# Optimization experiments

Measured on AMD Instinct MI355X. Metric: run time of the kernel, lower is better.

The kernel has to match this reference:

```python
import jax, jax.numpy as jnp
import numpy as np
import itertools

F = 3          # num_sparse_features
C = 256        # num_categories
D = 64         # embedding_dim
H = 1024       # hidden_units
ND = 13        # num_dense_features
B = 16384      # batch
COMBOS = [c for r in range(2, F + 1) for c in itertools.combinations(range(F), r)]
WIDE_DIM = C * F + sum(C ** len(c) for c in COMBOS) + ND
DEEP_IN = F * D + ND


def setup_inputs() -> dict:
    key = jax.random.key(0)
    ks = jax.random.split(key, 12)
    sparse_inputs = jax.random.randint(ks[0], (B, F), 0, C, dtype=jnp.int32)
    dense_inputs = jax.random.normal(ks[1], (B, ND), dtype=jnp.float32)
    wide_w = jax.random.normal(ks[2], (WIDE_DIM,), dtype=jnp.float32) * 0.01
    wide_b = jax.random.normal(ks[3], (1,), dtype=jnp.float32) * 0.01
    emb = jax.random.normal(ks[4], (F, C, D), dtype=jnp.float32) * 0.05
    W1 = jax.random.normal(ks[5], (H, DEEP_IN), dtype=jnp.float32) / np.sqrt(DEEP_IN).astype(np.float32)
    b1 = jnp.zeros((H,), jnp.float32)
    W2 = jax.random.normal(ks[6], (H, H), dtype=jnp.float32) / np.sqrt(H).astype(np.float32)
    b2 = jnp.zeros((H,), jnp.float32)
    W3 = jax.random.normal(ks[7], (1, H), dtype=jnp.float32) / np.sqrt(H).astype(np.float32)
    b3 = jnp.zeros((1,), jnp.float32)
    return {"sparse_inputs": sparse_inputs, "dense_inputs": dense_inputs,
            "wide_w": wide_w, "wide_b": wide_b, "emb": emb,
            "W1": W1, "b1": b1, "W2": W2, "b2": b2, "W3": W3, "b3": b3}


def reference(sparse_inputs, dense_inputs, wide_w, wide_b, emb, W1, b1, W2, b2, W3, b3):
    # Wide path: one_hot(x) @ W.T  ==  gather of W columns at the hot indices.
    wide = wide_b[0]  # scalar, broadcasts to [B]
    for i in range(F):  # per-feature one-hot block, width C each
        wide = wide + wide_w[i * C + sparse_inputs[:, i]]
    off = F * C
    for combo in COMBOS:  # cross-feature one-hot blocks, width C**len(combo)
        cross = sparse_inputs[:, combo[0]]
        for j in combo[1:]:
            # faithful to source: multiplies by num_sparse_features (F), not C
            cross = cross * F + sparse_inputs[:, j]
        wide = wide + wide_w[off + cross]
        off += C ** len(combo)
    wide = wide + dense_inputs @ wide_w[off:off + ND]  # dense tail of wide linear
    wide = wide[:, None]  # [B, 1]

    # Deep path: per-feature embedding lookup -> concat -> 3-layer MLP
    embedded = jnp.concatenate([emb[i][sparse_inputs[:, i]] for i in range(F)], axis=1)  # [B, F*D]
    deep_x = jnp.concatenate([embedded, dense_inputs], axis=1)  # [B, DEEP_IN]
    h = jax.nn.relu(deep_x @ W1.T + b1)
    h = jax.nn.relu(h @ W2.T + b2)
    deep = h @ W3.T + b3  # [B, 1]

    return jax.nn.sigmoid(wide + deep)
```

## Files before the change

kernel.cpp:

```cpp
#include <hip/hip_runtime.h>
#include <stdint.h>


#define BATCH 16384
#define HDIM 1024
#define KPAD 256
#define DEEP_IN 205

typedef short bf16x8 __attribute__((ext_vector_type(8)));
typedef float f32x4 __attribute__((ext_vector_type(4)));
typedef uint16_t u16x8 __attribute__((ext_vector_type(8)));

__device__ __forceinline__ float bf2f(uint16_t u) {
    uint32_t x = ((uint32_t)u) << 16;
    float f;
    __builtin_memcpy(&f, &x, 4);
    return f;
}

__device__ __forceinline__ uint16_t f2bf(float f) {
    uint32_t x;
    __builtin_memcpy(&x, &f, 4);
    uint32_t r = (x + 0x7fffu + ((x >> 16) & 1u)) >> 16;
    return (uint16_t)r;
}

__device__ __forceinline__ void async_ld16(const uint16_t* g, uint16_t* l) {
    __builtin_amdgcn_global_load_lds(
        (const __attribute__((address_space(1))) uint32_t*)g,
        (__attribute__((address_space(3))) uint32_t*)l, 16, 0, 0);
}

__global__ __launch_bounds__(256) void prep_kernel(
    const int* __restrict__ sp, const float* __restrict__ dense,
    const float* __restrict__ emb,
    const float* __restrict__ W1, const float* __restrict__ W2,
    const float* __restrict__ ww, const float* __restrict__ wb,
    uint16_t* __restrict__ dx, uint16_t* __restrict__ W1b,
    uint16_t* __restrict__ W2b, float* __restrict__ wide)
{
    const int bid = blockIdx.x;
    if (bid < 2048) {
        int idx = bid * 256 + threadIdx.x;
        int b = idx >> 5, c0 = (idx & 31) * 8;
        u16x8 o;
        if (c0 < 192) {
            int f = c0 >> 6, cc = c0 & 63;
            int s = sp[b * 3 + f];
            const float* e = emb + (size_t)(((f << 8) + s) * 64 + cc);
            float4 v0 = *(const float4*)e;
            float4 v1 = *(const float4*)(e + 4);
            o[0] = f2bf(v0.x); o[1] = f2bf(v0.y); o[2] = f2bf(v0.z); o[3] = f2bf(v0.w);
            o[4] = f2bf(v1.x); o[5] = f2bf(v1.y); o[6] = f2bf(v1.z); o[7] = f2bf(v1.w);
        } else {
#pragma unroll
            for (int t = 0; t < 8; t++) {
                int c = c0 + t;
                o[t] = (c >= 192 && c < DEEP_IN) ? f2bf(dense[b * 13 + (c - 192)])
                                                 : (uint16_t)0;
            }
        }
        *(u16x8*)(dx + (size_t)idx * 8) = o;
    } else if (bid < 2560) {
        int k = (bid - 2048) * 256 + threadIdx.x;
        const float* src = W2 + (size_t)k * 8;
        float4 v0 = *(const float4*)src;
        float4 v1 = *(const float4*)(src + 4);
        u16x8 o;
        o[0] = f2bf(v0.x); o[1] = f2bf(v0.y); o[2] = f2bf(v0.z); o[3] = f2bf(v0.w);
        o[4] = f2bf(v1.x); o[5] = f2bf(v1.y); o[6] = f2bf(v1.z); o[7] = f2bf(v1.w);
        *(u16x8*)(W2b + (size_t)k * 8) = o;
    } else if (bid < 2688) {
        int idx = (bid - 2560) * 256 + threadIdx.x;
        int n = idx >> 5, c0 = (idx & 31) * 8;
        u16x8 o;
#pragma unroll
        for (int t = 0; t < 8; t++) {
            int c = c0 + t;
            o[t] = (c < DEEP_IN) ? f2bf(W1[n * DEEP_IN + c]) : (uint16_t)0;
        }
        *(u16x8*)(W1b + (size_t)idx * 8) = o;
    } else {
        int b = (bid - 2688) * 256 + threadIdx.x;
        int s0 = sp[b * 3], s1 = sp[b * 3 + 1], s2 = sp[b * 3 + 2];
        float w = wb[0];
        w += ww[s0] + ww[256 + s1] + ww[512 + s2];
        w += ww[768    + s0 * 3 + s1];
        w += ww[66304  + s0 * 3 + s2];
        w += ww[131840 + s1 * 3 + s2];
        w += ww[197376 + (s0 * 3 + s1) * 3 + s2];
        const float* wd = ww + 16974592;
        float acc = 0.f;
#pragma unroll
        for (int j = 0; j < 13; j++) acc += dense[b * 13 + j] * wd[j];
        wide[b] = w + acc;
    }
}

__global__ __launch_bounds__(1024, 4) void gemm_bt(
    const uint16_t* __restrict__ A, const uint16_t* __restrict__ Bw,
    const float* __restrict__ bias, uint16_t* __restrict__ C,
    int M, int N, int K, int relu)
{
    __shared__ __align__(16) uint16_t Al[2][8192];
    __shared__ __align__(16) uint16_t Bl[2][8192];

    const int tid = threadIdx.x;
    const int lane = tid & 63;
    const int wave = tid >> 6;
    const int wm = wave >> 2;
    const int wn = wave & 3;

    const int id = blockIdx.x;
    const int xcd = id & 7;
    const int slot = id >> 3;
    const int mb8 = (M >> 8) >> 3;
    const int by = xcd * mb8 + (slot >> 2);
    const int bx = slot & 3;
    const int bm = by * 256;
    const int bn = bx * 256;
    const int rl = lane & 15, q = lane >> 4;

    f32x4 acc[4][4];
#pragma unroll
    for (int i = 0; i < 4; i++)
#pragma unroll
        for (int j = 0; j < 4; j++) acc[i][j] = (f32x4)0.f;

    const uint16_t* aS = A + (size_t)(bm + wave * 16 + rl) * K + q * 8;
    const uint16_t* bS = Bw + (size_t)(bn + wave * 16 + rl) * K + q * 8;
    const int dOf = wave * 512;

    async_ld16(aS, &Al[0][dOf]);
    async_ld16(bS, &Bl[0][dOf]);
    asm volatile("s_waitcnt vmcnt(0)" ::: "memory");
    __syncthreads();

    int p = 0;
    for (int k0 = 32; k0 < K; k0 += 32) {
        async_ld16(aS + k0, &Al[p ^ 1][dOf]);
        async_ld16(bS + k0, &Bl[p ^ 1][dOf]);

        bf16x8 af[4], bfr[4];
#pragma unroll
        for (int i = 0; i < 4; i++)
            af[i] = *(const bf16x8*)&Al[p][(wm * 4 + i) * 512 + lane * 8];
#pragma unroll
        for (int j = 0; j < 4; j++)
            bfr[j] = *(const bf16x8*)&Bl[p][(wn * 4 + j) * 512 + lane * 8];
#pragma unroll
        for (int i = 0; i < 4; i++)
#pragma unroll
            for (int j = 0; j < 4; j++)
                acc[i][j] = __builtin_amdgcn_mfma_f32_16x16x32_bf16(
                    af[i], bfr[j], acc[i][j], 0, 0, 0);

        asm volatile("s_waitcnt vmcnt(0)" ::: "memory");
        __syncthreads();
        p ^= 1;
    }

    {
        bf16x8 af[4], bfr[4];
#pragma unroll
        for (int i = 0; i < 4; i++)
            af[i] = *(const bf16x8*)&Al[p][(wm * 4 + i) * 512 + lane * 8];
#pragma unroll
        for (int j = 0; j < 4; j++)
            bfr[j] = *(const bf16x8*)&Bl[p][(wn * 4 + j) * 512 + lane * 8];
#pragma unroll
        for (int i = 0; i < 4; i++)
#pragma unroll
            for (int j = 0; j < 4; j++)
                acc[i][j] = __builtin_amdgcn_mfma_f32_16x16x32_bf16(
                    af[i], bfr[j], acc[i][j], 0, 0, 0);
    }

#pragma unroll
    for (int i = 0; i < 4; i++) {
#pragma unroll
        for (int j = 0; j < 4; j++) {
            int n = bn + (wn * 4 + j) * 16 + rl;
            float bv = bias[n];
#pragma unroll
            for (int r = 0; r < 4; r++) {
                int m = bm + (wm * 4 + i) * 16 + q * 4 + r;
                float v = acc[i][j][r] + bv;
                if (relu) v = fmaxf(v, 0.f);
                C[(size_t)m * N + n] = f2bf(v);
            }
        }
    }
}

__global__ __launch_bounds__(256) void final_kernel(
    const uint16_t* __restrict__ h2, const float* __restrict__ W3,
    const float* __restrict__ b3, const float* __restrict__ wide,
    float* __restrict__ out)
{
    int wave = threadIdx.x >> 6, lane = threadIdx.x & 63;
    int row = blockIdx.x * 4 + wave;
    const uint16_t* hr = h2 + (size_t)row * HDIM + lane * 16;
    u16x8 h0 = *(const u16x8*)hr;
    u16x8 h1 = *(const u16x8*)(hr + 8);
    const float* w3 = W3 + lane * 16;
    float s = 0.f;
#pragma unroll
    for (int t = 0; t < 8; t++) s += bf2f(h0[t]) * w3[t];
#pragma unroll
    for (int t = 0; t < 8; t++) s += bf2f(h1[t]) * w3[8 + t];
#pragma unroll
    for (int off = 32; off; off >>= 1) s += __shfl_down(s, off, 64);
    if (lane == 0) {
        float x = s + wide[row] + b3[0];
        out[row] = 1.f / (1.f + __expf(-x));
    }
}

extern "C" void kernel_launch(void* const* d_in, const int* in_sizes, int n_in,
                              void* d_out, int out_size, void* d_ws, size_t ws_size,
                              hipStream_t stream) {
    const int*   sp    = (const int*)d_in[0];
    const float* dense = (const float*)d_in[1];
    const float* ww    = (const float*)d_in[2];
    const float* wb    = (const float*)d_in[3];
    const float* emb   = (const float*)d_in[4];
    const float* W1    = (const float*)d_in[5];
    const float* b1    = (const float*)d_in[6];
    const float* W2    = (const float*)d_in[7];
    const float* b2    = (const float*)d_in[8];
    const float* W3    = (const float*)d_in[9];
    const float* b3    = (const float*)d_in[10];
    float* out = (float*)d_out;

    char* ws = (char*)d_ws;
    float*    wide = (float*)ws;
    uint16_t* dxp  = (uint16_t*)(ws + 65536);
    uint16_t* W1b  = (uint16_t*)(ws + 8454144);
    uint16_t* W2b  = (uint16_t*)(ws + 8978432);
    uint16_t* h1   = (uint16_t*)(ws + 11075584);
    uint16_t* h2   = (uint16_t*)(ws + 44630016);

    prep_kernel<<<2752, 256, 0, stream>>>(sp, dense, emb, W1, W2, ww, wb,
                                          dxp, W1b, W2b, wide);
    gemm_bt<<<(BATCH / 256) * 4, 1024, 0, stream>>>(
        dxp, W1b, b1, h1, BATCH, HDIM, KPAD, 1);
    gemm_bt<<<(BATCH / 256) * 4, 1024, 0, stream>>>(
        h1, W2b, b2, h2, BATCH, HDIM, HDIM, 1);
    final_kernel<<<BATCH / 4, 256, 0, stream>>>(h2, W3, b3, wide, out);
}
```

Before: 191.6 us.

## Fuse embedding gather into first GEMM and final projection into second GEMM epilogue

Removes the separate prep, first-GEMM, and final kernels. The first kernel now gathers embeddings, dense features and W1 straight into LDS as bf16 and computes layer 1 with K trimmed to 224. It also converts W2 and computes the wide term with b3 folded in. The second GEMM uses 128x256 tiles with 512 threads and folds relu, the W3 dot product and atomics into a per-row accumulator, so h2 is never written. A last-block counter then applies the sigmoid. This saves launches and the dx/h2 round trips, at the cost of float atomics, an uncoalesced W1 gather repeated per block, and a single block doing the final pass.

```diff
diff --git a/kernel.cpp b/kernel.cpp
--- a/kernel.cpp
+++ b/kernel.cpp
@@ -4,19 +4,12 @@
 
 #define BATCH 16384
 #define HDIM 1024
-#define KPAD 256
+#define K1 224
 #define DEEP_IN 205
 
 typedef short bf16x8 __attribute__((ext_vector_type(8)));
 typedef float f32x4 __attribute__((ext_vector_type(4)));
 typedef uint16_t u16x8 __attribute__((ext_vector_type(8)));
-
-__device__ __forceinline__ float bf2f(uint16_t u) {
-    uint32_t x = ((uint32_t)u) << 16;
-    float f;
-    __builtin_memcpy(&f, &x, 4);
-    return f;
-}
 
 __device__ __forceinline__ uint16_t f2bf(float f) {
     uint32_t x;
@@ -31,78 +24,151 @@
         (__attribute__((address_space(3))) uint32_t*)l, 16, 0, 0);
 }
 
-__global__ __launch_bounds__(256) void prep_kernel(
+__global__ __launch_bounds__(512, 4) void mega1(
     const int* __restrict__ sp, const float* __restrict__ dense,
-    const float* __restrict__ emb,
-    const float* __restrict__ W1, const float* __restrict__ W2,
+    const float* __restrict__ emb, const float* __restrict__ W1,
+    const float* __restrict__ b1, const float* __restrict__ W2,
     const float* __restrict__ ww, const float* __restrict__ wb,
-    uint16_t* __restrict__ dx, uint16_t* __restrict__ W1b,
-    uint16_t* __restrict__ W2b, float* __restrict__ wide)
+    const float* __restrict__ b3,
+    uint16_t* __restrict__ h1, uint16_t* __restrict__ W2b,
+    float* __restrict__ wide, unsigned* __restrict__ cnt)
 {
     const int bid = blockIdx.x;
-    if (bid < 2048) {
-        int idx = bid * 256 + threadIdx.x;
-        int b = idx >> 5, c0 = (idx & 31) * 8;
-        u16x8 o;
-        if (c0 < 192) {
-            int f = c0 >> 6, cc = c0 & 63;
-            int s = sp[b * 3 + f];
-            const float* e = emb + (size_t)(((f << 8) + s) * 64 + cc);
-            float4 v0 = *(const float4*)e;
-            float4 v1 = *(const float4*)(e + 4);
+    const int tid = threadIdx.x;
+
+    if (bid >= 512) {
+        if (bid < 768) {
+            int k = (bid - 512) * 512 + tid;
+            const float* src = W2 + (size_t)k * 8;
+            float4 v0 = *(const float4*)src;
+            float4 v1 = *(const float4*)(src + 4);
+            u16x8 o;
             o[0] = f2bf(v0.x); o[1] = f2bf(v0.y); o[2] = f2bf(v0.z); o[3] = f2bf(v0.w);
             o[4] = f2bf(v1.x); o[5] = f2bf(v1.y); o[6] = f2bf(v1.z); o[7] = f2bf(v1.w);
+            *(u16x8*)(W2b + (size_t)k * 8) = o;
         } else {
-#pragma unroll
-            for (int t = 0; t < 8; t++) {
-                int c = c0 + t;
-                o[t] = (c >= 192 && c < DEEP_IN) ? f2bf(dense[b * 13 + (c - 192)])
-                                                 : (uint16_t)0;
+            int b = (bid - 768) * 512 + tid;
+            int s0 = sp[b * 3], s1 = sp[b * 3 + 1], s2 = sp[b * 3 + 2];
+            float w = wb[0] + b3[0];
+            w += ww[s0] + ww[256 + s1] + ww[512 + s2];
+            w += ww[768    + s0 * 3 + s1];
+            w += ww[66304  + s0 * 3 + s2];
+            w += ww[131840 + s1 * 3 + s2];
+            w += ww[197376 + (s0 * 3 + s1) * 3 + s2];
+            const float* wd = ww + 16974592;
+            float acc = 0.f;
+#pragma unroll
+            for (int j = 0; j < 13; j++) acc += dense[b * 13 + j] * wd[j];
+            wide[b] = w + acc;
+            if (bid == 768 && tid == 0) *cnt = 0u;
+        }
+        return;
+    }
+
+    __shared__ __align__(16) uint16_t Al[4096];
+    __shared__ __align__(16) uint16_t Bl[8192];
+
+    const int lane = tid & 63;
+    const int wave = tid >> 6;
+    const int wm = wave >> 2;
+    const int wn = wave & 3;
+    const int xcd = bid & 7;
+    const int slot = bid >> 3;
+    const int by = xcd * 16 + (slot >> 2);
+    const int bx = slot & 3;
+    const int bm = by * 128;
+    const int bn = bx * 256;
+    const int rl = lane & 15, q = lane >> 4;
+
+    const int rA = bm + wave * 16 + rl;
+    const int s0 = sp[rA * 3], s1 = sp[rA * 3 + 1], s2 = sp[rA * 3 + 2];
+    const float* e0 = emb + (size_t)s0 * 64;
+    const float* e1 = emb + (size_t)(256 + s1) * 64;
+    const float* e2 = emb + (size_t)(512 + s2) * 64;
+    const float* dA = dense + (size_t)rA * 13;
+    const int n0 = bn + (2 * wave) * 16 + rl;
+    const float* w10 = W1 + (size_t)n0 * 205;
+    const float* w11 = w10 + (size_t)16 * 205;
+
+    f32x4 acc[4][4];
+#pragma unroll
+    for (int i = 0; i < 4; i++)
+#pragma unroll
+        for (int j = 0; j < 4; j++) acc[i][j] = (f32x4)0.f;
+
+    u16x8 a8, bb0, bb1;
+
+#define BUILD(K0)                                                              \
+    {                                                                          \
+        int x = (K0) + q * 8;                                                  \
+        if (x < 192) {                                                         \
+            const float* e = (x < 64) ? (e0 + x)                               \
+                           : (x < 128) ? (e1 + (x - 64)) : (e2 + (x - 128));   \
+            float4 v0 = *(const float4*)e;                                     \
+            float4 v1 = *(const float4*)(e + 4);                               \
+            a8[0] = f2bf(v0.x); a8[1] = f2bf(v0.y);                            \
+            a8[2] = f2bf(v0.z); a8[3] = f2bf(v0.w);                            \
+            a8[4] = f2bf(v1.x); a8[5] = f2bf(v1.y);                            \
+            a8[6] = f2bf(v1.z); a8[7] = f2bf(v1.w);                            \
+        } else {                                                               \
+            _Pragma("unroll") for (int t = 0; t < 8; t++) {                    \
+                int c = x + t;                                                 \
+                a8[t] = (c < DEEP_IN) ? f2bf(dA[c - 192]) : (uint16_t)0;       \
+            }                                                                  \
+        }                                                                      \
+        _Pragma("unroll") for (int t = 0; t < 8; t++) {                        \
+            int c = x + t;                                                     \
+            bb0[t] = (c < DEEP_IN) ? f2bf(w10[c]) : (uint16_t)0;               \
+            bb1[t] = (c < DEEP_IN) ? f2bf(w11[c]) : (uint16_t)0;               \
+        }                                                                      \
+    }
+
+    BUILD(0)
+    for (int k0 = 0; k0 < K1; k0 += 32) {
+        __syncthreads();
+        *(u16x8*)&Al[wave * 512 + lane * 8] = a8;
+        *(u16x8*)&Bl[(2 * wave) * 512 + lane * 8] = bb0;
+        *(u16x8*)&Bl[(2 * wave + 1) * 512 + lane * 8] = bb1;
+        __syncthreads();
+        if (k0 + 32 < K1) BUILD(k0 + 32)
+        bf16x8 af[4], bfr[4];
+#pragma unroll
+        for (int i = 0; i < 4; i++)
+            af[i] = *(const bf16x8*)&Al[(wm * 4 + i) * 512 + lane * 8];
+#pragma unroll
+        for (int j = 0; j < 4; j++)
+            bfr[j] = *(const bf16x8*)&Bl[(wn * 4 + j) * 512 + lane * 8];
+#pragma unroll
+        for (int i = 0; i < 4; i++)
+#pragma unroll
+            for (int j = 0; j < 4; j++)
+                acc[i][j] = __builtin_amdgcn_mfma_f32_16x16x32_bf16(
+                    af[i], bfr[j], acc[i][j], 0, 0, 0);
+    }
+#undef BUILD
+
+#pragma unroll
+    for (int i = 0; i < 4; i++) {
+#pragma unroll
+        for (int j = 0; j < 4; j++) {
+            int n = bn + (wn * 4 + j) * 16 + rl;
+            float bv = b1[n];
+#pragma unroll
+            for (int r = 0; r < 4; r++) {
+                int m = bm + (wm * 4 + i) * 16 + q * 4 + r;
+                h1[(size_t)m * HDIM + n] = f2bf(fmaxf(acc[i][j][r] + bv, 0.f));
             }
         }
-        *(u16x8*)(dx + (size_t)idx * 8) = o;
-    } else if (bid < 2560) {
-        int k = (bid - 2048) * 256 + threadIdx.x;
-        const float* src = W2 + (size_t)k * 8;
-        float4 v0 = *(const float4*)src;
-        float4 v1 = *(const float4*)(src + 4);
-        u16x8 o;
-        o[0] = f2bf(v0.x); o[1] = f2bf(v0.y); o[2] = f2bf(v0.z); o[3] = f2bf(v0.w);
-        o[4] = f2bf(v1.x); o[5] = f2bf(v1.y); o[6] = f2bf(v1.z); o[7] = f2bf(v1.w);
-        *(u16x8*)(W2b + (size_t)k * 8) = o;
-    } else if (bid < 2688) {
-        int idx = (bid - 2560) * 256 + threadIdx.x;
-        int n = idx >> 5, c0 = (idx & 31) * 8;
-        u16x8 o;
-#pragma unroll
-        for (int t = 0; t < 8; t++) {
-            int c = c0 + t;
-            o[t] = (c < DEEP_IN) ? f2bf(W1[n * DEEP_IN + c]) : (uint16_t)0;
-        }
-        *(u16x8*)(W1b + (size_t)idx * 8) = o;
-    } else {
-        int b = (bid - 2688) * 256 + threadIdx.x;
-        int s0 = sp[b * 3], s1 = sp[b * 3 + 1], s2 = sp[b * 3 + 2];
-        float w = wb[0];
-        w += ww[s0] + ww[256 + s1] + ww[512 + s2];
-        w += ww[768    + s0 * 3 + s1];
-        w += ww[66304  + s0 * 3 + s2];
-        w += ww[131840 + s1 * 3 + s2];
-        w += ww[197376 + (s0 * 3 + s1) * 3 + s2];
-        const float* wd = ww + 16974592;
-        float acc = 0.f;
-#pragma unroll
-        for (int j = 0; j < 13; j++) acc += dense[b * 13 + j] * wd[j];
-        wide[b] = w + acc;
-    }
-}
-
-__global__ __launch_bounds__(1024, 4) void gemm_bt(
+    }
+}
+
+__global__ __launch_bounds__(512, 4) void gemm2(
     const uint16_t* __restrict__ A, const uint16_t* __restrict__ Bw,
-    const float* __restrict__ bias, uint16_t* __restrict__ C,
-    int M, int N, int K, int relu)
+    const float* __restrict__ bias, const float* __restrict__ W3,
+    float* __restrict__ outacc, float* __restrict__ out,
+    unsigned* __restrict__ cnt)
 {
-    __shared__ __align__(16) uint16_t Al[2][8192];
+    __shared__ __align__(16) uint16_t Al[2][4096];
     __shared__ __align__(16) uint16_t Bl[2][8192];
 
     const int tid = threadIdx.x;
@@ -110,16 +176,15 @@
     const int wave = tid >> 6;
     const int wm = wave >> 2;
     const int wn = wave & 3;
-
     const int id = blockIdx.x;
     const int xcd = id & 7;
     const int slot = id >> 3;
-    const int mb8 = (M >> 8) >> 3;
-    const int by = xcd * mb8 + (slot >> 2);
+    const int by = xcd * 16 + (slot >> 2);
     const int bx = slot & 3;
-    const int bm = by * 256;
+    const int bm = by * 128;
     const int bn = bx * 256;
     const int rl = lane & 15, q = lane >> 4;
+    const int K = HDIM;
 
     f32x4 acc[4][4];
 #pragma unroll
@@ -128,18 +193,21 @@
         for (int j = 0; j < 4; j++) acc[i][j] = (f32x4)0.f;
 
     const uint16_t* aS = A + (size_t)(bm + wave * 16 + rl) * K + q * 8;
-    const uint16_t* bS = Bw + (size_t)(bn + wave * 16 + rl) * K + q * 8;
-    const int dOf = wave * 512;
-
-    async_ld16(aS, &Al[0][dOf]);
-    async_ld16(bS, &Bl[0][dOf]);
+    const uint16_t* bS0 = Bw + (size_t)(bn + wave * 32 + rl) * K + q * 8;
+    const uint16_t* bS1 = bS0 + (size_t)16 * K;
+    const int dA = wave * 512, dB0 = wave * 1024, dB1 = wave * 1024 + 512;
+
+    async_ld16(aS, &Al[0][dA]);
+    async_ld16(bS0, &Bl[0][dB0]);
+    async_ld16(bS1, &Bl[0][dB1]);
     asm volatile("s_waitcnt vmcnt(0)" ::: "memory");
     __syncthreads();
 
     int p = 0;
     for (int k0 = 32; k0 < K; k0 += 32) {
-        async_ld16(aS + k0, &Al[p ^ 1][dOf]);
-        async_ld16(bS + k0, &Bl[p ^ 1][dOf]);
+        async_ld16(aS + k0, &Al[p ^ 1][dA]);
+        async_ld16(bS0 + k0, &Bl[p ^ 1][dB0]);
+        async_ld16(bS1 + k0, &Bl[p ^ 1][dB1]);
 
         bf16x8 af[4], bfr[4];
 #pragma unroll
@@ -159,7 +227,6 @@
         __syncthreads();
         p ^= 1;
     }
-
     {
         bf16x8 af[4], bfr[4];
 #pragma unroll
@@ -176,44 +243,46 @@
                     af[i], bfr[j], acc[i][j], 0, 0, 0);
     }
 
+    float bv[4], w3v[4];
+#pragma unroll
+    for (int j = 0; j < 4; j++) {
+        int n = bn + (wn * 4 + j) * 16 + rl;
+        bv[j] = bias[n];
+        w3v[j] = W3[n];
+    }
 #pragma unroll
     for (int i = 0; i < 4; i++) {
 #pragma unroll
-        for (int j = 0; j < 4; j++) {
-            int n = bn + (wn * 4 + j) * 16 + rl;
-            float bv = bias[n];
-#pragma unroll
-            for (int r = 0; r < 4; r++) {
+        for (int r = 0; r < 4; r++) {
+            float pt = 0.f;
+#pragma unroll
+            for (int j = 0; j < 4; j++)
+                pt += fmaxf(acc[i][j][r] + bv[j], 0.f) * w3v[j];
+            pt += __shfl_xor(pt, 1);
+            pt += __shfl_xor(pt, 2);
+            pt += __shfl_xor(pt, 4);
+            pt += __shfl_xor(pt, 8);
+            if (rl == 0) {
                 int m = bm + (wm * 4 + i) * 16 + q * 4 + r;
-                float v = acc[i][j][r] + bv;
-                if (relu) v = fmaxf(v, 0.f);
-                C[(size_t)m * N + n] = f2bf(v);
+                atomicAdd(&outacc[m], pt);
             }
         }
     }
-}
-
-__global__ __launch_bounds__(256) void final_kernel(
-    const uint16_t* __restrict__ h2, const float* __restrict__ W3,
-    const float* __restrict__ b3, const float* __restrict__ wide,
-    float* __restrict__ out)
-{
-    int wave = threadIdx.x >> 6, lane = threadIdx.x & 63;
-    int row = blockIdx.x * 4 + wave;
-    const uint16_t* hr = h2 + (size_t)row * HDIM + lane * 16;
-    u16x8 h0 = *(const u16x8*)hr;
-    u16x8 h1 = *(const u16x8*)(hr + 8);
-    const float* w3 = W3 + lane * 16;
-    float s = 0.f;
-#pragma unroll
-    for (int t = 0; t < 8; t++) s += bf2f(h0[t]) * w3[t];
-#pragma unroll
-    for (int t = 0; t < 8; t++) s += bf2f(h1[t]) * w3[8 + t];
-#pragma unroll
-    for (int off = 32; off; off >>= 1) s += __shfl_down(s, off, 64);
-    if (lane == 0) {
-        float x = s + wide[row] + b3[0];
-        out[row] = 1.f / (1.f + __expf(-x));
+
+    __threadfence();
+    __syncthreads();
+    __shared__ unsigned lastv;
+    if (tid == 0) {
+        lastv = __hip_atomic_fetch_add(cnt, 1u, __ATOMIC_ACQ_REL,
+                                       __HIP_MEMORY_SCOPE_AGENT);
+    }
+    __syncthreads();
+    if (lastv == 511u) {
+        for (int i2 = tid; i2 < BATCH; i2 += 512) {
+            float v = __hip_atomic_load(&outacc[i2], __ATOMIC_RELAXED,
+                                        __HIP_MEMORY_SCOPE_AGENT);
+            out[i2] = 1.f / (1.f + __expf(-v));
+        }
     }
 }
 
@@ -234,18 +303,12 @@
     float* out = (float*)d_out;
 
     char* ws = (char*)d_ws;
-    float*    wide = (float*)ws;
-    uint16_t* dxp  = (uint16_t*)(ws + 65536);
-    uint16_t* W1b  = (uint16_t*)(ws + 8454144);
-    uint16_t* W2b  = (uint16_t*)(ws + 8978432);
-    uint16_t* h1   = (uint16_t*)(ws + 11075584);
-    uint16_t* h2   = (uint16_t*)(ws + 44630016);
-
-    prep_kernel<<<2752, 256, 0, stream>>>(sp, dense, emb, W1, W2, ww, wb,
-                                          dxp, W1b, W2b, wide);
-    gemm_bt<<<(BATCH / 256) * 4, 1024, 0, stream>>>(
-        dxp, W1b, b1, h1, BATCH, HDIM, KPAD, 1);
-    gemm_bt<<<(BATCH / 256) * 4, 1024, 0, stream>>>(
-        h1, W2b, b2, h2, BATCH, HDIM, HDIM, 1);
-    final_kernel<<<BATCH / 4, 256, 0, stream>>>(h2, W3, b3, wide, out);
-}
+    unsigned* cnt  = (unsigned*)ws;
+    float*    wide = (float*)(ws + 4096);
+    uint16_t* W2b  = (uint16_t*)(ws + 69632);
+    uint16_t* h1   = (uint16_t*)(ws + 2166784);
+
+    mega1<<<800, 512, 0, stream>>>(sp, dense, emb, W1, b1, W2, ww, wb, b3,
+                                   h1, W2b, wide, cnt);
+    gemm2<<<512, 512, 0, stream>>>(h1, W2b, b2, W3, wide, out, cnt);
+}
```

Result: slower. 257.5 us (+34.4%).

## Fuse final W3 dot into second GEMM epilogue and shrink GEMM tiles

Applied to the files above, without the earlier changes.

The second GEMM's epilogue now applies bias and ReLU, multiplies by W3, reduces across lanes and atomically adds per-row partials into the wide buffer. This removes the h2 write and reread, and a small sigmoid kernel finishes the job. Both GEMMs switch to 128x256 tiles with 512 threads. The fused GEMM reads A fragments directly from global memory rather than staging them in LDS, and runs K in steps of 64. The trade-offs are float atomics, which make the summation order nondeterministic, and uncoalesced direct A loads that could stall the MFMA pipeline.

```diff
diff --git a/kernel.cpp b/kernel.cpp
--- a/kernel.cpp
+++ b/kernel.cpp
@@ -10,13 +10,6 @@
 typedef short bf16x8 __attribute__((ext_vector_type(8)));
 typedef float f32x4 __attribute__((ext_vector_type(4)));
 typedef uint16_t u16x8 __attribute__((ext_vector_type(8)));
-
-__device__ __forceinline__ float bf2f(uint16_t u) {
-    uint32_t x = ((uint32_t)u) << 16;
-    float f;
-    __builtin_memcpy(&f, &x, 4);
-    return f;
-}
 
 __device__ __forceinline__ uint16_t f2bf(float f) {
     uint32_t x;
@@ -36,6 +29,7 @@
     const float* __restrict__ emb,
     const float* __restrict__ W1, const float* __restrict__ W2,
     const float* __restrict__ ww, const float* __restrict__ wb,
+    const float* __restrict__ b3,
     uint16_t* __restrict__ dx, uint16_t* __restrict__ W1b,
     uint16_t* __restrict__ W2b, float* __restrict__ wide)
 {
@@ -83,7 +77,7 @@
     } else {
         int b = (bid - 2688) * 256 + threadIdx.x;
         int s0 = sp[b * 3], s1 = sp[b * 3 + 1], s2 = sp[b * 3 + 2];
-        float w = wb[0];
+        float w = wb[0] + b3[0];
         w += ww[s0] + ww[256 + s1] + ww[512 + s2];
         w += ww[768    + s0 * 3 + s1];
         w += ww[66304  + s0 * 3 + s2];
@@ -97,12 +91,12 @@
     }
 }
 
-__global__ __launch_bounds__(1024, 4) void gemm_bt(
+__global__ __launch_bounds__(512, 4) void gemm_relu(
     const uint16_t* __restrict__ A, const uint16_t* __restrict__ Bw,
     const float* __restrict__ bias, uint16_t* __restrict__ C,
-    int M, int N, int K, int relu)
+    int M, int N, int K)
 {
-    __shared__ __align__(16) uint16_t Al[2][8192];
+    __shared__ __align__(16) uint16_t Al[2][4096];
     __shared__ __align__(16) uint16_t Bl[2][8192];
 
     const int tid = threadIdx.x;
@@ -110,14 +104,13 @@
     const int wave = tid >> 6;
     const int wm = wave >> 2;
     const int wn = wave & 3;
-
     const int id = blockIdx.x;
     const int xcd = id & 7;
     const int slot = id >> 3;
-    const int mb8 = (M >> 8) >> 3;
-    const int by = xcd * mb8 + (slot >> 2);
+    const int mbX = (M >> 7) >> 3;
+    const int by = xcd * mbX + (slot >> 2);
     const int bx = slot & 3;
-    const int bm = by * 256;
+    const int bm = by * 128;
     const int bn = bx * 256;
     const int rl = lane & 15, q = lane >> 4;
 
@@ -128,18 +121,21 @@
         for (int j = 0; j < 4; j++) acc[i][j] = (f32x4)0.f;
 
     const uint16_t* aS = A + (size_t)(bm + wave * 16 + rl) * K + q * 8;
-    const uint16_t* bS = Bw + (size_t)(bn + wave * 16 + rl) * K + q * 8;
-    const int dOf = wave * 512;
-
-    async_ld16(aS, &Al[0][dOf]);
-    async_ld16(bS, &Bl[0][dOf]);
+    const uint16_t* bS0 = Bw + (size_t)(bn + wave * 32 + rl) * K + q * 8;
+    const uint16_t* bS1 = bS0 + (size_t)16 * K;
+    const int dA = wave * 512, dB0 = wave * 1024, dB1 = wave * 1024 + 512;
+
+    async_ld16(aS, &Al[0][dA]);
+    async_ld16(bS0, &Bl[0][dB0]);
+    async_ld16(bS1, &Bl[0][dB1]);
     asm volatile("s_waitcnt vmcnt(0)" ::: "memory");
     __syncthreads();
 
     int p = 0;
     for (int k0 = 32; k0 < K; k0 += 32) {
-        async_ld16(aS + k0, &Al[p ^ 1][dOf]);
-        async_ld16(bS + k0, &Bl[p ^ 1][dOf]);
+        async_ld16(aS + k0, &Al[p ^ 1][dA]);
+        async_ld16(bS0 + k0, &Bl[p ^ 1][dB0]);
+        async_ld16(bS1 + k0, &Bl[p ^ 1][dB1]);
 
         bf16x8 af[4], bfr[4];
 #pragma unroll
@@ -159,7 +155,6 @@
         __syncthreads();
         p ^= 1;
     }
-
     {
         bf16x8 af[4], bfr[4];
 #pragma unroll
@@ -185,36 +180,129 @@
 #pragma unroll
             for (int r = 0; r < 4; r++) {
                 int m = bm + (wm * 4 + i) * 16 + q * 4 + r;
-                float v = acc[i][j][r] + bv;
-                if (relu) v = fmaxf(v, 0.f);
+                float v = fmaxf(acc[i][j][r] + bv, 0.f);
                 C[(size_t)m * N + n] = f2bf(v);
             }
         }
     }
 }
 
-__global__ __launch_bounds__(256) void final_kernel(
-    const uint16_t* __restrict__ h2, const float* __restrict__ W3,
-    const float* __restrict__ b3, const float* __restrict__ wide,
-    float* __restrict__ out)
+__global__ __launch_bounds__(512, 4) void gemm_fused(
+    const uint16_t* __restrict__ A, const uint16_t* __restrict__ Bw,
+    const float* __restrict__ bias, const float* __restrict__ W3,
+    float* __restrict__ outacc, int M, int N, int K)
 {
-    int wave = threadIdx.x >> 6, lane = threadIdx.x & 63;
-    int row = blockIdx.x * 4 + wave;
-    const uint16_t* hr = h2 + (size_t)row * HDIM + lane * 16;
-    u16x8 h0 = *(const u16x8*)hr;
-    u16x8 h1 = *(const u16x8*)(hr + 8);
-    const float* w3 = W3 + lane * 16;
-    float s = 0.f;
-#pragma unroll
-    for (int t = 0; t < 8; t++) s += bf2f(h0[t]) * w3[t];
-#pragma unroll
-    for (int t = 0; t < 8; t++) s += bf2f(h1[t]) * w3[8 + t];
-#pragma unroll
-    for (int off = 32; off; off >>= 1) s += __shfl_down(s, off, 64);
-    if (lane == 0) {
-        float x = s + wide[row] + b3[0];
-        out[row] = 1.f / (1.f + __expf(-x));
-    }
+    __shared__ __align__(16) uint16_t Bl[2][16384];
+
+    const int tid = threadIdx.x;
+    const int lane = tid & 63;
+    const int wave = tid >> 6;
+    const int wm = wave >> 2;
+    const int wn = wave & 3;
+    const int id = blockIdx.x;
+    const int xcd = id & 7;
+    const int slot = id >> 3;
+    const int mbX = (M >> 7) >> 3;
+    const int by = xcd * mbX + (slot >> 2);
+    const int bx = slot & 3;
+    const int bm = by * 128;
+    const int bn = bx * 256;
+    const int rl = lane & 15, q = lane >> 4;
+
+    f32x4 acc[4][4];
+#pragma unroll
+    for (int i = 0; i < 4; i++)
+#pragma unroll
+        for (int j = 0; j < 4; j++) acc[i][j] = (f32x4)0.f;
+
+    const uint16_t* bS0 = Bw + (size_t)(bn + wave * 32 + rl) * K + q * 8;
+    const uint16_t* bS1 = bS0 + (size_t)16 * K;
+    const int dB0 = (2 * wave) * 1024, dB1 = (2 * wave + 1) * 1024;
+    const uint16_t* aP = A + (size_t)(bm + wm * 64 + rl) * K + q * 8;
+    const size_t rs16 = (size_t)16 * K;
+
+    async_ld16(bS0,      &Bl[0][dB0]);
+    async_ld16(bS0 + 32, &Bl[0][dB0 + 512]);
+    async_ld16(bS1,      &Bl[0][dB1]);
+    async_ld16(bS1 + 32, &Bl[0][dB1 + 512]);
+
+    const int niter = K >> 6;
+    for (int k = 0; k < niter; ++k) {
+        asm volatile("s_waitcnt vmcnt(0)" ::: "memory");
+        asm volatile("s_barrier" ::: "memory");
+        const int p = k & 1;
+        if (k + 1 < niter) {
+            const int ko = (k + 1) << 6;
+            async_ld16(bS0 + ko,      &Bl[p ^ 1][dB0]);
+            async_ld16(bS0 + ko + 32, &Bl[p ^ 1][dB0 + 512]);
+            async_ld16(bS1 + ko,      &Bl[p ^ 1][dB1]);
+            async_ld16(bS1 + ko + 32, &Bl[p ^ 1][dB1 + 512]);
+        }
+        const int ka = k << 6;
+        {
+            bf16x8 af[4], bfr[4];
+#pragma unroll
+            for (int i = 0; i < 4; i++)
+                af[i] = *(const bf16x8*)(aP + (size_t)i * rs16 + ka);
+#pragma unroll
+            for (int j = 0; j < 4; j++)
+                bfr[j] = *(const bf16x8*)&Bl[p][(wn * 4 + j) * 1024 + lane * 8];
+#pragma unroll
+            for (int i = 0; i < 4; i++)
+#pragma unroll
+                for (int j = 0; j < 4; j++)
+                    acc[i][j] = __builtin_amdgcn_mfma_f32_16x16x32_bf16(
+                        af[i], bfr[j], acc[i][j], 0, 0, 0);
+        }
+        {
+            bf16x8 af[4], bfr[4];
+#pragma unroll
+            for (int i = 0; i < 4; i++)
+                af[i] = *(const bf16x8*)(aP + (size_t)i * rs16 + ka + 32);
+#pragma unroll
+            for (int j = 0; j < 4; j++)
+                bfr[j] = *(const bf16x8*)&Bl[p][(wn * 4 + j) * 1024 + 512 + lane * 8];
+#pragma unroll
+            for (int i = 0; i < 4; i++)
+#pragma unroll
+                for (int j = 0; j < 4; j++)
+                    acc[i][j] = __builtin_amdgcn_mfma_f32_16x16x32_bf16(
+                        af[i], bfr[j], acc[i][j], 0, 0, 0);
+        }
+    }
+
+    float bv[4], w3v[4];
+#pragma unroll
+    for (int j = 0; j < 4; j++) {
+        int n = bn + (wn * 4 + j) * 16 + rl;
+        bv[j] = bias[n];
+        w3v[j] = W3[n];
+    }
+#pragma unroll
+    for (int i = 0; i < 4; i++) {
+#pragma unroll
+        for (int r = 0; r < 4; r++) {
+            float pt = 0.f;
+#pragma unroll
+            for (int j = 0; j < 4; j++)
+                pt += fmaxf(acc[i][j][r] + bv[j], 0.f) * w3v[j];
+            pt += __shfl_xor(pt, 1);
+            pt += __shfl_xor(pt, 2);
+            pt += __shfl_xor(pt, 4);
+            pt += __shfl_xor(pt, 8);
+            if (rl == 0) {
+                int m = bm + (wm * 4 + i) * 16 + q * 4 + r;
+                atomicAdd(&outacc[m], pt);
+            }
+        }
+    }
+}
+
+__global__ __launch_bounds__(256) void sigmoid_kernel(
+    const float* __restrict__ outacc, float* __restrict__ out)
+{
+    int b = blockIdx.x * 256 + threadIdx.x;
+    out[b] = 1.f / (1.f + __expf(-outacc[b]));
 }
 
 extern "C" void kernel_launch(void* const* d_in, const int* in_sizes, int n_in,
@@ -239,13 +327,12 @@
     uint16_t* W1b  = (uint16_t*)(ws + 8454144);
     uint16_t* W2b  = (uint16_t*)(ws + 8978432);
     uint16_t* h1   = (uint16_t*)(ws + 11075584);
-    uint16_t* h2   = (uint16_t*)(ws + 44630016);
-
-    prep_kernel<<<2752, 256, 0, stream>>>(sp, dense, emb, W1, W2, ww, wb,
+
+    prep_kernel<<<2752, 256, 0, stream>>>(sp, dense, emb, W1, W2, ww, wb, b3,
                                           dxp, W1b, W2b, wide);
-    gemm_bt<<<(BATCH / 256) * 4, 1024, 0, stream>>>(
-        dxp, W1b, b1, h1, BATCH, HDIM, KPAD, 1);
-    gemm_bt<<<(BATCH / 256) * 4, 1024, 0, stream>>>(
-        h1, W2b, b2, h2, BATCH, HDIM, HDIM, 1);
-    final_kernel<<<BATCH / 4, 256, 0, stream>>>(h2, W3, b3, wide, out);
-}
+    gemm_relu<<<(BATCH / 128) * 4, 512, 0, stream>>>(
+        dxp, W1b, b1, h1, BATCH, HDIM, KPAD);
+    gemm_fused<<<(BATCH / 128) * 4, 512, 0, stream>>>(
+        h1, W2b, b2, W3, wide, BATCH, HDIM, HDIM);
+    sigmoid_kernel<<<BATCH / 256, 256, 0, stream>>>(wide, out);
+}
```

New measurement: 226.4 us. 18.2% more time.
